# Kernel tuning notes

Hardware: AMD Instinct MI355X
Metric: run time of the kernel (lower is better)

Reference implementation:

```python
import jax, jax.numpy as jnp
import numpy as np
from jax import lax

DN = ('NHWC', 'HWIO', 'NHWC')

def _conv(x, w):
    return lax.conv_general_dilated(x, w, window_strides=(1, 1), padding='SAME', dimension_numbers=DN)

def _hard_sigmoid(z):
    # keras hard_sigmoid: clip(0.2*z + 0.5, 0, 1) -- default recurrent_activation of ConvLSTM2D
    return jnp.clip(0.2 * z + 0.5, 0.0, 1.0)

def setup_inputs() -> dict:
    key = jax.random.key(0)
    ks = jax.random.split(key, 6)
    B, T, H, W, Cin = 4, 16, 64, 64, 32
    F, kh, kw = 64, 3, 3
    x  = jax.random.normal(ks[0], (B, T, H, W, Cin), dtype=jnp.float32)
    Wx = jax.random.normal(ks[1], (kh, kw, Cin, 4 * F), dtype=jnp.float32) * 0.05
    Wh = jax.random.normal(ks[2], (kh, kw, F, 4 * F), dtype=jnp.float32) * 0.05
    b  = jnp.zeros((4 * F,), dtype=jnp.float32)
    Wp = jax.random.normal(ks[3], (1, 1, Cin, F), dtype=jnp.float32) * 0.05
    bp = jnp.zeros((F,), dtype=jnp.float32)
    return {"x": x, "Wx": Wx, "Wh": Wh, "b": b, "Wp": Wp, "bp": bp}

def reference(x, Wx, Wh, b, Wp, bp):
    B, T, H, W, Cin = x.shape
    F = Wh.shape[2]
    # Precompute the input-to-gate convolutions for all timesteps at once.
    zx = _conv(x.reshape(B * T, H, W, Cin), Wx) + b          # (B*T, H, W, 4F)
    zx = zx.reshape(B, T, H, W, 4 * F).transpose(1, 0, 2, 3, 4)  # time-major

    def step(carry, zx_t):
        h, c = carry
        z = zx_t + _conv(h, Wh)                              # (B, H, W, 4F)
        zi, zf, zc, zo = jnp.split(z, 4, axis=-1)            # keras gate order i,f,c,o
        i = _hard_sigmoid(zi)
        f = _hard_sigmoid(zf)
        c_new = f * c + i * jnp.tanh(zc)
        o = _hard_sigmoid(zo)
        h_new = o * jnp.tanh(c_new)
        return (h_new, c_new), h_new

    h0 = jnp.zeros((B, H, W, F), dtype=x.dtype)
    c0 = jnp.zeros((B, H, W, F), dtype=x.dtype)
    _, hs = lax.scan(step, (h0, c0), zx)                     # (T, B, H, W, F)
    convlstm_out = hs.transpose(1, 0, 2, 3, 4)               # (B, T, H, W, F)

    # TimeDistributed 1x1 projection of the input as the residual branch.
    residual = _conv(x.reshape(B * T, H, W, Cin), Wp) + bp
    residual = residual.reshape(B, T, H, W, F)
    return convlstm_out + residual
```

## Files before the change

### kernel.cpp

```cpp
#include <hip/hip_runtime.h>

#define B_ 4
#define T_ 16
#define H_ 64
#define W_ 64
#define CIN 32
#define F_ 64
#define NCH 256
#define KSTEPS 27
#define TSLAB (H_ * W_ * F_)

#define OFF_H0 557056
#define OFF_H1 2654208

typedef __attribute__((ext_vector_type(8))) short short8;
typedef __attribute__((ext_vector_type(4))) float floatx4;
typedef __attribute__((address_space(3))) unsigned int  lds_u32;
typedef __attribute__((address_space(1))) const unsigned int g_u32;

__device__ __forceinline__ unsigned short f2bf(float f) {
  union { float f; unsigned u; } v; v.f = f;
  unsigned r = v.u + 0x7FFFu + ((v.u >> 16) & 1u);
  return (unsigned short)(r >> 16);
}

__device__ __forceinline__ float tanh_fast(float z) {
  float e = __expf(2.0f * z);
  return 1.0f - 2.0f * __builtin_amdgcn_rcpf(e + 1.0f);
}

__global__ void prep_weights(const float* __restrict__ Wx, const float* __restrict__ Wh,
                             unsigned short* __restrict__ WT) {
  int idx = blockIdx.x * 256 + threadIdx.x;
  int s = idx / 10240;
  int r = idx - s * 10240;
  int n = r / 40;
  int c = r - n * 40;
  unsigned short v = 0;
  if (c < 32) {
    int k  = s * 32 + c;
    int g  = k / 96;
    int ch = k - g * 96;
    float f = (ch < CIN) ? Wx[(g * CIN + ch) * NCH + n]
                         : Wh[(g * F_ + (ch - CIN)) * NCH + n];
    v = f2bf(f);
  }
  WT[idx] = v;
}

__global__ void prep_zero_h(float4* __restrict__ p) {
  int idx = blockIdx.x * 256 + threadIdx.x;
  p[idx] = make_float4(0.f, 0.f, 0.f, 0.f);
}

__global__ void prep_zero_c(float* __restrict__ out) {
  int idx = blockIdx.x * 256 + threadIdx.x;
  int b = idx >> 16;
  int i = idx & 65535;
  ((float4*)(out + (size_t)b * (T_ * TSLAB)))[i] = make_float4(0.f, 0.f, 0.f, 0.f);
}

__device__ __forceinline__ void stage_wt(const unsigned short* __restrict__ src,
                                         short* dstbuf, int w, int lane) {
  __attribute__((address_space(3))) unsigned short* d =
      (__attribute__((address_space(3))) unsigned short*)dstbuf + w * 2560;
  const unsigned short* s = src + w * 2560 + lane * 8;
  #pragma unroll
  for (int q = 0; q < 5; q++)
    __builtin_amdgcn_global_load_lds((g_u32*)(s + q * 512), (lds_u32*)(d + q * 512),
                                     16, 0, 0);
}

__global__ __launch_bounds__(256, 1)
void step_kernel(const float* __restrict__ x, const float* __restrict__ bias,
                 const float* __restrict__ Wp, const float* __restrict__ bp,
                 const unsigned short* __restrict__ WT,
                 const unsigned short* __restrict__ hprev,
                 unsigned short* __restrict__ hnew,
                 float* __restrict__ out, int t)
{
  __shared__ __align__(16) char smem[77824];
  short* patch = (short*)smem;
  short* bl0   = (short*)(smem + 28288);
  short* bl1   = (short*)(smem + 48768);
  float* gact  = (float*)smem;
  float* WpL   = (float*)(smem + 69632);

  const int tid  = threadIdx.x;
  const int w    = tid >> 6;
  const int lane = tid & 63;
  const int quad = lane >> 4;
  const int lr   = lane & 15;

  const int bid = blockIdx.x;
  const int b   = bid >> 6;
  const int rem = bid & 63;
  const int y0  = (rem >> 1) << 1;
  const int x0  = (rem & 1) << 5;

  stage_wt(WT, bl0, w, lane);

  if (tid < 136) {
    int sy = tid / 34, sx = tid - sy * 34;
    int yy = y0 + sy - 1, xx = x0 + sx - 1;
    short* dst = patch + tid * 104;
    if (yy >= 0 && yy < H_ && xx >= 0 && xx < W_) {
      const float4* xs = (const float4*)(x + ((((b * T_ + t) * H_ + yy) * W_ + xx) * CIN));
      #pragma unroll
      for (int j = 0; j < 4; j++) {
        float4 f0 = xs[2 * j];
        float4 f1 = xs[2 * j + 1];
        union { short8 v; unsigned short u[8]; } pk;
        pk.u[0] = f2bf(f0.x); pk.u[1] = f2bf(f0.y); pk.u[2] = f2bf(f0.z); pk.u[3] = f2bf(f0.w);
        pk.u[4] = f2bf(f1.x); pk.u[5] = f2bf(f1.y); pk.u[6] = f2bf(f1.z); pk.u[7] = f2bf(f1.w);
        ((short8*)dst)[j] = pk.v;
      }
      const uint4* hs = (const uint4*)(hprev + ((b * H_ + yy) * W_ + xx) * F_);
      uint4* d2 = (uint4*)(dst + 32);
      #pragma unroll
      for (int j = 0; j < 8; j++) d2[j] = hs[j];
    } else {
      uint4 z = make_uint4(0, 0, 0, 0);
      uint4* d4 = (uint4*)dst;
      #pragma unroll
      for (int j = 0; j < 12; j++) d4[j] = z;
    }
  }

  float bias_r[4];
  #pragma unroll
  for (int nf = 0; nf < 4; nf++) bias_r[nf] = bias[w * 64 + nf * 16 + lr];

  floatx4 acc[4][4];
  #pragma unroll
  for (int mf = 0; mf < 4; mf++)
    #pragma unroll
    for (int nf = 0; nf < 4; nf++)
      acc[mf][nf] = (floatx4){0.f, 0.f, 0.f, 0.f};

  __syncthreads();

  const unsigned short* wsrc = WT + 10240;
  for (int s = 0; s < KSTEPS; s++) {
    short* cur = (s & 1) ? bl1 : bl0;
    if (s < KSTEPS - 1) {
      stage_wt(wsrc, (s & 1) ? bl0 : bl1, w, lane);
      wsrc += 10240;
    }
    int g  = s / 3;
    int c0 = (s - g * 3) * 32;
    int dy = g / 3, dx = g - dy * 3;
    short8 afr[4], bfr[4];
    #pragma unroll
    for (int mf = 0; mf < 4; mf++) {
      int p  = mf * 16 + lr;
      int ty = p >> 5, tx = p & 31;
      afr[mf] = *(const short8*)(patch + ((ty + dy) * 34 + tx + dx) * 104 + c0 + quad * 8);
    }
    #pragma unroll
    for (int nf = 0; nf < 4; nf++) {
      int n = w * 64 + nf * 16 + lr;
      bfr[nf] = *(const short8*)(cur + n * 40 + quad * 8);
    }
    #pragma unroll
    for (int mf = 0; mf < 4; mf++)
      #pragma unroll
      for (int nf = 0; nf < 4; nf++)
        acc[mf][nf] = __builtin_amdgcn_mfma_f32_16x16x32_bf16(afr[mf], bfr[nf], acc[mf][nf], 0, 0, 0);
    __syncthreads();
  }

  #pragma unroll
  for (int mf = 0; mf < 4; mf++)
    #pragma unroll
    for (int nf = 0; nf < 4; nf++)
      #pragma unroll
      for (int r = 0; r < 4; r++) {
        int mm = mf * 16 + quad * 4 + r;
        float z = acc[mf][nf][r] + bias_r[nf];
        float a;
        if (w == 2) a = tanh_fast(z);
        else {
          a = __builtin_fmaf(z, 0.2f, 0.5f);
          a = fminf(fmaxf(a, 0.f), 1.f);
        }
        gact[(w * 64 + mm) * 68 + nf * 16 + lr] = a;
      }
  {
    float4* d = (float4*)WpL;
    const float4* sWp = (const float4*)Wp;
    d[tid * 2]     = sWp[tid * 2];
    d[tid * 2 + 1] = sWp[tid * 2 + 1];
  }

  const int mloc = tid >> 2;
  const int cb   = (tid & 3) * 16;
  const int tyo  = mloc >> 5, txo = mloc & 31;
  const int gy   = y0 + tyo, gx = x0 + txo;
  const int hbase   = ((b * H_ + gy) * W_ + gx) * F_ + cb;
  const int outbase = (((b * T_ + t) * H_ + gy) * W_ + gx) * F_ + cb;

  float xv[32];
  {
    const float4* xs = (const float4*)(x + ((((b * T_ + t) * H_ + gy) * W_ + gx) * CIN));
    #pragma unroll
    for (int j = 0; j < 8; j++) {
      float4 f = xs[j];
      xv[4 * j] = f.x; xv[4 * j + 1] = f.y; xv[4 * j + 2] = f.z; xv[4 * j + 3] = f.w;
    }
  }
  float4 co4[4];
  #pragma unroll
  for (int j = 0; j < 4; j++) co4[j] = *(const float4*)(out + outbase + 4 * j);

  __syncthreads();

  float res[16];
  #pragma unroll
  for (int j = 0; j < 16; j++) res[j] = bp[cb + j];
  for (int ci = 0; ci < 32; ci++) {
    float xf = xv[ci];
    #pragma unroll
    for (int j4 = 0; j4 < 4; j4++) {
      float4 wv = *(const float4*)(WpL + ci * 64 + cb + j4 * 4);
      res[j4 * 4 + 0] += xf * wv.x;
      res[j4 * 4 + 1] += xf * wv.y;
      res[j4 * 4 + 2] += xf * wv.z;
      res[j4 * 4 + 3] += xf * wv.w;
    }
  }

  union { unsigned short hv[16]; uint4 q[2]; } hu;
  #pragma unroll
  for (int j4 = 0; j4 < 4; j4++) {
    int jj = j4 * 4;
    float4 gi = *(const float4*)(gact + (0 * 64 + mloc) * 68 + cb + jj);
    float4 gf = *(const float4*)(gact + (1 * 64 + mloc) * 68 + cb + jj);
    float4 gg = *(const float4*)(gact + (2 * 64 + mloc) * 68 + cb + jj);
    float4 go = *(const float4*)(gact + (3 * 64 + mloc) * 68 + cb + jj);
    float cold[4] = {co4[j4].x, co4[j4].y, co4[j4].z, co4[j4].w};
    float iv[4] = {gi.x, gi.y, gi.z, gi.w};
    float fv[4] = {gf.x, gf.y, gf.z, gf.w};
    float gv[4] = {gg.x, gg.y, gg.z, gg.w};
    float ov[4] = {go.x, go.y, go.z, go.w};
    float cn4[4], h4[4];
    #pragma unroll
    for (int e = 0; e < 4; e++) {
      float cn = fv[e] * cold[e] + iv[e] * gv[e];
      float h  = ov[e] * tanh_fast(cn);
      cn4[e] = cn; h4[e] = h;
      hu.hv[jj + e] = f2bf(h);
    }
    if (t < T_ - 1)
      *(float4*)(out + outbase + TSLAB + jj) = make_float4(cn4[0], cn4[1], cn4[2], cn4[3]);
    *(float4*)(out + outbase + jj) = make_float4(h4[0] + res[jj + 0], h4[1] + res[jj + 1],
                                                 h4[2] + res[jj + 2], h4[3] + res[jj + 3]);
  }
  uint4* hd = (uint4*)(hnew + hbase);
  hd[0] = hu.q[0];
  hd[1] = hu.q[1];
}

extern "C" void kernel_launch(void* const* d_in, const int* in_sizes, int n_in,
                              void* d_out, int out_size, void* d_ws, size_t ws_size,
                              hipStream_t stream) {
  const float* x    = (const float*)d_in[0];
  const float* Wx   = (const float*)d_in[1];
  const float* Wh   = (const float*)d_in[2];
  const float* bias = (const float*)d_in[3];
  const float* Wp   = (const float*)d_in[4];
  const float* bp   = (const float*)d_in[5];
  float* out = (float*)d_out;

  unsigned short* WT = (unsigned short*)d_ws;
  unsigned short* h0 = (unsigned short*)((char*)d_ws + OFF_H0);
  unsigned short* h1 = (unsigned short*)((char*)d_ws + OFF_H1);

  hipLaunchKernelGGL(prep_weights, dim3(1080), dim3(256), 0, stream, Wx, Wh, WT);
  hipLaunchKernelGGL(prep_zero_h, dim3(1024), dim3(256), 0, stream,
                     (float4*)((char*)d_ws + OFF_H0));
  hipLaunchKernelGGL(prep_zero_c, dim3(1024), dim3(256), 0, stream, out);

  for (int t = 0; t < T_; t++) {
    const unsigned short* hp = (t & 1) ? h1 : h0;
    unsigned short*       hn = (t & 1) ? h0 : h1;
    hipLaunchKernelGGL(step_kernel, dim3(256), dim3(256), 0, stream,
                       x, bias, Wp, bp, WT, hp, hn, out, t);
  }
}
```

Baseline: 710.3 us.

## Halve spatial tile to 2x16 pixels, launch 512 blocks with smaller LDS footprint

Changes each step-kernel block to cover 32 pixels instead of 64, doubling the grid to 512 blocks on a 256-CU GPU so that every CU has work. Shrinks the weight-row padding from 40 to 36 shorts, cuts LDS to about 51 KB and raises launch bounds so several blocks can share a CU. It also splits the patch load across two threads per pixel and remaps block IDs by batch stride. The cost is that each block re-stages the full weight set for half as many pixels, which doubles weight traffic per output and adds more halo overhead.

Result: slower. 1.036 ms (+45.8%).

```diff
diff --git a/kernel.cpp b/kernel.cpp
--- a/kernel.cpp
+++ b/kernel.cpp
@@ -8,6 +8,7 @@
 #define F_ 64
 #define NCH 256
 #define KSTEPS 27
+#define WSTEP 9216
 #define TSLAB (H_ * W_ * F_)
 
 #define OFF_H0 557056
@@ -32,10 +33,10 @@
 __global__ void prep_weights(const float* __restrict__ Wx, const float* __restrict__ Wh,
                              unsigned short* __restrict__ WT) {
   int idx = blockIdx.x * 256 + threadIdx.x;
-  int s = idx / 10240;
-  int r = idx - s * 10240;
-  int n = r / 40;
-  int c = r - n * 40;
+  int s = idx / WSTEP;
+  int r = idx - s * WSTEP;
+  int n = r / 36;
+  int c = r - n * 36;
   unsigned short v = 0;
   if (c < 32) {
     int k  = s * 32 + c;
@@ -63,15 +64,22 @@
 __device__ __forceinline__ void stage_wt(const unsigned short* __restrict__ src,
                                          short* dstbuf, int w, int lane) {
   __attribute__((address_space(3))) unsigned short* d =
-      (__attribute__((address_space(3))) unsigned short*)dstbuf + w * 2560;
-  const unsigned short* s = src + w * 2560 + lane * 8;
-  #pragma unroll
-  for (int q = 0; q < 5; q++)
+      (__attribute__((address_space(3))) unsigned short*)dstbuf;
+  const unsigned short* s = src + lane * 8;
+  #pragma unroll
+  for (int i = 0; i < 4; i++) {
+    int q = w + 4 * i;
     __builtin_amdgcn_global_load_lds((g_u32*)(s + q * 512), (lds_u32*)(d + q * 512),
                                      16, 0, 0);
-}
-
-__global__ __launch_bounds__(256, 1)
+  }
+  if (w < 2) {
+    int q = w + 16;
+    __builtin_amdgcn_global_load_lds((g_u32*)(s + q * 512), (lds_u32*)(d + q * 512),
+                                     16, 0, 0);
+  }
+}
+
+__global__ __launch_bounds__(256, 3)
 void step_kernel(const float* __restrict__ x, const float* __restrict__ bias,
                  const float* __restrict__ Wp, const float* __restrict__ bp,
                  const unsigned short* __restrict__ WT,
@@ -79,12 +87,12 @@
                  unsigned short* __restrict__ hnew,
                  float* __restrict__ out, int t)
 {
-  __shared__ __align__(16) char smem[77824];
+  __shared__ __align__(16) char smem[51840];
   short* patch = (short*)smem;
-  short* bl0   = (short*)(smem + 28288);
-  short* bl1   = (short*)(smem + 48768);
+  short* bl0   = (short*)(smem + 14976);
+  short* bl1   = (short*)(smem + 33408);
   float* gact  = (float*)smem;
-  float* WpL   = (float*)(smem + 69632);
+  float* WpL   = (float*)(smem + 34816);
 
   const int tid  = threadIdx.x;
   const int w    = tid >> 6;
@@ -92,38 +100,50 @@
   const int quad = lane >> 4;
   const int lr   = lane & 15;
 
-  const int bid = blockIdx.x;
-  const int b   = bid >> 6;
-  const int rem = bid & 63;
-  const int y0  = (rem >> 1) << 1;
-  const int x0  = (rem & 1) << 5;
+  const int raw = blockIdx.x;
+  const int bid = (raw & 7) * 64 + (raw >> 3);
+  const int b   = bid >> 7;
+  const int rem = bid & 127;
+  const int y0  = (rem >> 2) << 1;
+  const int x0  = (rem & 3) << 4;
 
   stage_wt(WT, bl0, w, lane);
 
-  if (tid < 136) {
-    int sy = tid / 34, sx = tid - sy * 34;
+  if (tid < 144) {
+    int e = tid >> 1, half = tid & 1;
+    int sy = e / 18, sx = e - sy * 18;
     int yy = y0 + sy - 1, xx = x0 + sx - 1;
-    short* dst = patch + tid * 104;
-    if (yy >= 0 && yy < H_ && xx >= 0 && xx < W_) {
-      const float4* xs = (const float4*)(x + ((((b * T_ + t) * H_ + yy) * W_ + xx) * CIN));
-      #pragma unroll
-      for (int j = 0; j < 4; j++) {
-        float4 f0 = xs[2 * j];
-        float4 f1 = xs[2 * j + 1];
-        union { short8 v; unsigned short u[8]; } pk;
-        pk.u[0] = f2bf(f0.x); pk.u[1] = f2bf(f0.y); pk.u[2] = f2bf(f0.z); pk.u[3] = f2bf(f0.w);
-        pk.u[4] = f2bf(f1.x); pk.u[5] = f2bf(f1.y); pk.u[6] = f2bf(f1.z); pk.u[7] = f2bf(f1.w);
-        ((short8*)dst)[j] = pk.v;
+    short* dst = patch + e * 104;
+    bool in = (yy >= 0 && yy < H_ && xx >= 0 && xx < W_);
+    if (half == 0) {
+      if (in) {
+        const float4* xs = (const float4*)(x + ((((b * T_ + t) * H_ + yy) * W_ + xx) * CIN));
+        #pragma unroll
+        for (int j = 0; j < 4; j++) {
+          float4 f0 = xs[2 * j];
+          float4 f1 = xs[2 * j + 1];
+          union { short8 v; unsigned short u[8]; } pk;
+          pk.u[0] = f2bf(f0.x); pk.u[1] = f2bf(f0.y); pk.u[2] = f2bf(f0.z); pk.u[3] = f2bf(f0.w);
+          pk.u[4] = f2bf(f1.x); pk.u[5] = f2bf(f1.y); pk.u[6] = f2bf(f1.z); pk.u[7] = f2bf(f1.w);
+          ((short8*)dst)[j] = pk.v;
+        }
+      } else {
+        uint4 z = make_uint4(0, 0, 0, 0);
+        uint4* d4 = (uint4*)dst;
+        #pragma unroll
+        for (int j = 0; j < 4; j++) d4[j] = z;
       }
-      const uint4* hs = (const uint4*)(hprev + ((b * H_ + yy) * W_ + xx) * F_);
+    } else {
       uint4* d2 = (uint4*)(dst + 32);
-      #pragma unroll
-      for (int j = 0; j < 8; j++) d2[j] = hs[j];
-    } else {
-      uint4 z = make_uint4(0, 0, 0, 0);
-      uint4* d4 = (uint4*)dst;
-      #pragma unroll
-      for (int j = 0; j < 12; j++) d4[j] = z;
+      if (in) {
+        const uint4* hs = (const uint4*)(hprev + ((b * H_ + yy) * W_ + xx) * F_);
+        #pragma unroll
+        for (int j = 0; j < 8; j++) d2[j] = hs[j];
+      } else {
+        uint4 z = make_uint4(0, 0, 0, 0);
+        #pragma unroll
+        for (int j = 0; j < 8; j++) d2[j] = z;
+      }
     }
   }
 
@@ -131,39 +151,34 @@
   #pragma unroll
   for (int nf = 0; nf < 4; nf++) bias_r[nf] = bias[w * 64 + nf * 16 + lr];
 
-  floatx4 acc[4][4];
-  #pragma unroll
-  for (int mf = 0; mf < 4; mf++)
+  floatx4 acc[2][4];
+  #pragma unroll
+  for (int mf = 0; mf < 2; mf++)
     #pragma unroll
     for (int nf = 0; nf < 4; nf++)
       acc[mf][nf] = (floatx4){0.f, 0.f, 0.f, 0.f};
 
   __syncthreads();
 
-  const unsigned short* wsrc = WT + 10240;
+  const unsigned short* wsrc = WT + WSTEP;
   for (int s = 0; s < KSTEPS; s++) {
     short* cur = (s & 1) ? bl1 : bl0;
     if (s < KSTEPS - 1) {
       stage_wt(wsrc, (s & 1) ? bl0 : bl1, w, lane);
-      wsrc += 10240;
+      wsrc += WSTEP;
     }
     int g  = s / 3;
     int c0 = (s - g * 3) * 32;
     int dy = g / 3, dx = g - dy * 3;
-    short8 afr[4], bfr[4];
-    #pragma unroll
-    for (int mf = 0; mf < 4; mf++) {
-      int p  = mf * 16 + lr;
-      int ty = p >> 5, tx = p & 31;
-      afr[mf] = *(const short8*)(patch + ((ty + dy) * 34 + tx + dx) * 104 + c0 + quad * 8);
-    }
-    #pragma unroll
-    for (int nf = 0; nf < 4; nf++) {
-      int n = w * 64 + nf * 16 + lr;
-      bfr[nf] = *(const short8*)(cur + n * 40 + quad * 8);
-    }
-    #pragma unroll
-    for (int mf = 0; mf < 4; mf++)
+    short8 afr[2], bfr[4];
+    #pragma unroll
+    for (int mf = 0; mf < 2; mf++)
+      afr[mf] = *(const short8*)(patch + ((mf + dy) * 18 + lr + dx) * 104 + c0 + quad * 8);
+    #pragma unroll
+    for (int nf = 0; nf < 4; nf++)
+      bfr[nf] = *(const short8*)(cur + (w * 64 + nf * 16 + lr) * 36 + quad * 8);
+    #pragma unroll
+    for (int mf = 0; mf < 2; mf++)
       #pragma unroll
       for (int nf = 0; nf < 4; nf++)
         acc[mf][nf] = __builtin_amdgcn_mfma_f32_16x16x32_bf16(afr[mf], bfr[nf], acc[mf][nf], 0, 0, 0);
@@ -171,7 +186,7 @@
   }
 
   #pragma unroll
-  for (int mf = 0; mf < 4; mf++)
+  for (int mf = 0; mf < 2; mf++)
     #pragma unroll
     for (int nf = 0; nf < 4; nf++)
       #pragma unroll
@@ -184,7 +199,7 @@
           a = __builtin_fmaf(z, 0.2f, 0.5f);
           a = fminf(fmaxf(a, 0.f), 1.f);
         }
-        gact[(w * 64 + mm) * 68 + nf * 16 + lr] = a;
+        gact[(w * 32 + mm) * 68 + nf * 16 + lr] = a;
       }
   {
     float4* d = (float4*)WpL;
@@ -193,9 +208,9 @@
     d[tid * 2 + 1] = sWp[tid * 2 + 1];
   }
 
-  const int mloc = tid >> 2;
-  const int cb   = (tid & 3) * 16;
-  const int tyo  = mloc >> 5, txo = mloc & 31;
+  const int mloc = tid >> 3;
+  const int cb   = (tid & 7) * 8;
+  const int tyo  = mloc >> 4, txo = mloc & 15;
   const int gy   = y0 + tyo, gx = x0 + txo;
   const int hbase   = ((b * H_ + gy) * W_ + gx) * F_ + cb;
   const int outbase = (((b * T_ + t) * H_ + gy) * W_ + gx) * F_ + cb;
@@ -209,35 +224,32 @@
       xv[4 * j] = f.x; xv[4 * j + 1] = f.y; xv[4 * j + 2] = f.z; xv[4 * j + 3] = f.w;
     }
   }
-  float4 co4[4];
-  #pragma unroll
-  for (int j = 0; j < 4; j++) co4[j] = *(const float4*)(out + outbase + 4 * j);
+  float4 co4[2];
+  co4[0] = *(const float4*)(out + outbase);
+  co4[1] = *(const float4*)(out + outbase + 4);
 
   __syncthreads();
 
-  float res[16];
-  #pragma unroll
-  for (int j = 0; j < 16; j++) res[j] = bp[cb + j];
+  float res[8];
+  #pragma unroll
+  for (int j = 0; j < 8; j++) res[j] = bp[cb + j];
+  #pragma unroll
   for (int ci = 0; ci < 32; ci++) {
     float xf = xv[ci];
-    #pragma unroll
-    for (int j4 = 0; j4 < 4; j4++) {
-      float4 wv = *(const float4*)(WpL + ci * 64 + cb + j4 * 4);
-      res[j4 * 4 + 0] += xf * wv.x;
-      res[j4 * 4 + 1] += xf * wv.y;
-      res[j4 * 4 + 2] += xf * wv.z;
-      res[j4 * 4 + 3] += xf * wv.w;
-    }
-  }
-
-  union { unsigned short hv[16]; uint4 q[2]; } hu;
-  #pragma unroll
-  for (int j4 = 0; j4 < 4; j4++) {
+    float4 w0 = *(const float4*)(WpL + ci * 64 + cb);
+    float4 w1 = *(const float4*)(WpL + ci * 64 + cb + 4);
+    res[0] += xf * w0.x; res[1] += xf * w0.y; res[2] += xf * w0.z; res[3] += xf * w0.w;
+    res[4] += xf * w1.x; res[5] += xf * w1.y; res[6] += xf * w1.z; res[7] += xf * w1.w;
+  }
+
+  union { unsigned short hv[8]; uint4 q; } hu;
+  #pragma unroll
+  for (int j4 = 0; j4 < 2; j4++) {
     int jj = j4 * 4;
-    float4 gi = *(const float4*)(gact + (0 * 64 + mloc) * 68 + cb + jj);
-    float4 gf = *(const float4*)(gact + (1 * 64 + mloc) * 68 + cb + jj);
-    float4 gg = *(const float4*)(gact + (2 * 64 + mloc) * 68 + cb + jj);
-    float4 go = *(const float4*)(gact + (3 * 64 + mloc) * 68 + cb + jj);
+    float4 gi = *(const float4*)(gact + (0 * 32 + mloc) * 68 + cb + jj);
+    float4 gf = *(const float4*)(gact + (1 * 32 + mloc) * 68 + cb + jj);
+    float4 gg = *(const float4*)(gact + (2 * 32 + mloc) * 68 + cb + jj);
+    float4 go = *(const float4*)(gact + (3 * 32 + mloc) * 68 + cb + jj);
     float cold[4] = {co4[j4].x, co4[j4].y, co4[j4].z, co4[j4].w};
     float iv[4] = {gi.x, gi.y, gi.z, gi.w};
     float fv[4] = {gf.x, gf.y, gf.z, gf.w};
@@ -256,9 +268,7 @@
     *(float4*)(out + outbase + jj) = make_float4(h4[0] + res[jj + 0], h4[1] + res[jj + 1],
                                                  h4[2] + res[jj + 2], h4[3] + res[jj + 3]);
   }
-  uint4* hd = (uint4*)(hnew + hbase);
-  hd[0] = hu.q[0];
-  hd[1] = hu.q[1];
+  *(uint4*)(hnew + hbase) = hu.q;
 }
 
 extern "C" void kernel_launch(void* const* d_in, const int* in_sizes, int n_in,
@@ -276,7 +286,7 @@
   unsigned short* h0 = (unsigned short*)((char*)d_ws + OFF_H0);
   unsigned short* h1 = (unsigned short*)((char*)d_ws + OFF_H1);
 
-  hipLaunchKernelGGL(prep_weights, dim3(1080), dim3(256), 0, stream, Wx, Wh, WT);
+  hipLaunchKernelGGL(prep_weights, dim3(972), dim3(256), 0, stream, Wx, Wh, WT);
   hipLaunchKernelGGL(prep_zero_h, dim3(1024), dim3(256), 0, stream,
                      (float4*)((char*)d_ws + OFF_H0));
   hipLaunchKernelGGL(prep_zero_c, dim3(1024), dim3(256), 0, stream, out);
@@ -284,7 +294,7 @@
   for (int t = 0; t < T_; t++) {
     const unsigned short* hp = (t & 1) ? h1 : h0;
     unsigned short*       hn = (t & 1) ? h0 : h1;
-    hipLaunchKernelGGL(step_kernel, dim3(256), dim3(256), 0, stream,
+    hipLaunchKernelGGL(step_kernel, dim3(512), dim3(256), 0, stream,
                        x, bias, Wp, bp, WT, hp, hn, out, t);
   }
 }
```
